# Performance work log

Hardware: AMD Instinct MI355X
Metric: run time of the kernel (lower is better)

The kernel has to match this reference:

```python
import jax, jax.numpy as jnp
import numpy as np

NEIGHBOR_NUM = 4
POOLING_RATE = 4


def setup_inputs() -> dict:
    key = jax.random.key(0)
    k1, k2, k3 = jax.random.split(key, 3)
    B, N, C = 4, 8192, 256
    vertices = jax.random.normal(k1, (B, N, 3), dtype=jnp.float32)
    feature_map = jax.random.normal(k2, (B, N, C), dtype=jnp.float32)
    pool_num = N // POOLING_RATE
    sample_idx = jax.random.permutation(k3, N)[:pool_num].astype(jnp.int32)  # torch.randperm(N)[:pool_num]
    return {"vertices": vertices, "feature_map": feature_map, "radius": 1, "sample_idx": sample_idx}


def _query_ball_point(radius, nsample, xyz):
    # xyz: [B, N, 3]; self-query (new_xyz == xyz)
    B, N, _ = xyz.shape
    sq = jnp.sum(xyz * xyz, axis=-1)                       # [B, N]
    dist = -2.0 * jnp.einsum('bnc,bmc->bnm', xyz, xyz)     # [B, N, N]
    dist = dist + sq[:, :, None] + sq[:, None, :]
    # original code zeroes the diagonal (self-distance)
    diag = jnp.arange(N)
    dist = dist.at[:, diag, diag].set(0.0)
    # mark out-of-ball entries with sentinel N, sort indices, keep first nsample
    idx = jnp.arange(N, dtype=jnp.int32)
    group_idx = jnp.where(dist > radius ** 2, jnp.int32(N), idx[None, None, :])  # [B, N, N]
    group_idx = jnp.sort(group_idx, axis=-1)[:, :, :nsample]                     # [B, N, nsample]
    group_first = group_idx[:, :, :1]
    group_idx = jnp.where(group_idx == N, group_first, group_idx)
    return group_idx


def reference(vertices, feature_map, radius, sample_idx):
    B, N, _ = vertices.shape
    neighbor_index = _query_ball_point(radius, NEIGHBOR_NUM, vertices)          # [B, N, k]
    bidx = jnp.arange(B)[:, None, None]
    neighbor_feature = feature_map[bidx, neighbor_index]                        # [B, N, k, C]
    pooled_feature = jnp.max(neighbor_feature, axis=2)                          # [B, N, C]
    vertices_pool = vertices[:, sample_idx, :]                                  # [B, pool, 3]
    feature_map_pool = pooled_feature[:, sample_idx, :]                         # [B, pool, C]
    return (vertices_pool, feature_map_pool)
```

## Files before the change

kernel.cpp:

```cpp
#include <hip/hip_runtime.h>


#define BB 4
#define NN 8192
#define CC 256
#define PP 2048
#define KK 4
#define SS 1024
#define CH2 16

__device__ __forceinline__ float dist_ref(float xn0, float xn1, float xn2, float sqn,
                                          float x0, float x1, float x2) {
    const float sqm = __fadd_rn(__fadd_rn(__fmul_rn(x0, x0), __fmul_rn(x1, x1)),
                                __fmul_rn(x2, x2));
    const float dot = __fadd_rn(__fadd_rn(__fmul_rn(xn0, x0), __fmul_rn(xn1, x1)),
                                __fmul_rn(xn2, x2));
    return __fadd_rn(__fadd_rn(__fmul_rn(-2.0f, dot), sqn), sqm);
}

__global__ __launch_bounds__(256) void pool_layer_kernel(
    const float* __restrict__ vertices,
    const float* __restrict__ feat,
    const int*   __restrict__ radius_p,
    const int*   __restrict__ sample_idx,
    float* __restrict__ out_v,
    float* __restrict__ out_f)
{
    __shared__ float s_v[SS * 3];

    const int tid  = threadIdx.x;
    const int wave = tid >> 6;
    const int lane = tid & 63;
    const int q    = blockIdx.x * 4 + wave;
    const int b    = q >> 11;
    const int i    = q & (PP - 1);
    const float* vb = vertices + (size_t)b * NN * 3;

    const float4* v4 = (const float4*)vb;
    const float4 st0 = v4[tid];
    const float4 st1 = v4[tid + 256];
    const float4 st2 = v4[tid + 512];

    const int n = sample_idx[i];
    const float xn0 = vb[n * 3 + 0];
    const float xn1 = vb[n * 3 + 1];
    const float xn2 = vb[n * 3 + 2];
    const float sqn = __fadd_rn(__fadd_rn(__fmul_rn(xn0, xn0), __fmul_rn(xn1, xn1)),
                                __fmul_rn(xn2, xn2));
    const int   r  = radius_p[0];
    const float r2 = (float)(r * r);

    ((float4*)s_v)[tid]       = st0;
    ((float4*)s_v)[tid + 256] = st1;
    ((float4*)s_v)[tid + 512] = st2;

    if (lane < 3) out_v[((size_t)b * PP + i) * 3 + lane] = vb[n * 3 + lane];

    __syncthreads();

    int c0 = 0, c1 = 0, c2 = 0, c3 = 0, cnt = 0;
    #pragma unroll
    for (int c = 0; c < SS / 64; ++c) {
        const int m = c * 64 + lane;
        const float x0 = s_v[m * 3 + 0];
        const float x1 = s_v[m * 3 + 1];
        const float x2 = s_v[m * 3 + 2];
        const float dist = dist_ref(xn0, xn1, xn2, sqn, x0, x1, x2);
        unsigned long long mask = __ballot((m == n) || !(dist > r2));
        while (mask && cnt < KK) {
            const int v = c * 64 + (__ffsll(mask) - 1);
            c3 = (cnt == 3) ? v : c3;
            c2 = (cnt == 2) ? v : c2;
            c1 = (cnt == 1) ? v : c1;
            c0 = (cnt == 0) ? v : c0;
            ++cnt;
            mask &= (mask - 1);
        }
    }

    if (cnt < KK) {
        int l0 = NN, l1 = NN, l2 = NN, l3 = NN, lcnt = 0;
        int tot = 0;
        for (int base = 0; base < NN && tot < KK; base += 64 * CH2) {
            float qx[CH2], qy[CH2], qz[CH2];
            #pragma unroll
            for (int c = 0; c < CH2; ++c) {
                const int m = base + c * 64 + lane;
                qx[c] = vb[m * 3 + 0];
                qy[c] = vb[m * 3 + 1];
                qz[c] = vb[m * 3 + 2];
            }
            #pragma unroll
            for (int c = 0; c < CH2; ++c) {
                const int m = base + c * 64 + lane;
                const float dist = dist_ref(xn0, xn1, xn2, sqn, qx[c], qy[c], qz[c]);
                const bool hit = (m == n) || !(dist > r2);
                tot += (int)__popcll(__ballot(hit));
                if (hit && lcnt < KK) {
                    l3 = (lcnt == 3) ? m : l3;
                    l2 = (lcnt == 2) ? m : l2;
                    l1 = (lcnt == 1) ? m : l1;
                    l0 = (lcnt == 0) ? m : l0;
                    ++lcnt;
                }
            }
        }
        int g[KK];
        #pragma unroll
        for (int round = 0; round < KK; ++round) {
            int mmin = l0;
            #pragma unroll
            for (int off = 32; off > 0; off >>= 1)
                mmin = min(mmin, __shfl_xor(mmin, off));
            g[round] = mmin;
            if (l0 == mmin) { l0 = l1; l1 = l2; l2 = l3; l3 = NN; }
        }
        c0 = g[0];
        c1 = (g[1] == NN) ? g[0] : g[1];
        c2 = (g[2] == NN) ? g[0] : g[2];
        c3 = (g[3] == NN) ? g[0] : g[3];
    }

    const float4 a0 = ((const float4*)(feat + ((size_t)b * NN + c0) * CC))[lane];
    const float4 a1 = ((const float4*)(feat + ((size_t)b * NN + c1) * CC))[lane];
    const float4 a2 = ((const float4*)(feat + ((size_t)b * NN + c2) * CC))[lane];
    const float4 a3 = ((const float4*)(feat + ((size_t)b * NN + c3) * CC))[lane];
    float4 o;
    o.x = fmaxf(fmaxf(a0.x, a1.x), fmaxf(a2.x, a3.x));
    o.y = fmaxf(fmaxf(a0.y, a1.y), fmaxf(a2.y, a3.y));
    o.z = fmaxf(fmaxf(a0.z, a1.z), fmaxf(a2.z, a3.z));
    o.w = fmaxf(fmaxf(a0.w, a1.w), fmaxf(a2.w, a3.w));
    ((float4*)(out_f + ((size_t)b * PP + i) * CC))[lane] = o;
}

extern "C" void kernel_launch(void* const* d_in, const int* in_sizes, int n_in,
                              void* d_out, int out_size, void* d_ws, size_t ws_size,
                              hipStream_t stream) {
    const float* vertices   = (const float*)d_in[0];
    const float* feat       = (const float*)d_in[1];
    const int*   radius_p   = (const int*)d_in[2];
    const int*   sample_idx = (const int*)d_in[3];

    float* out_v = (float*)d_out;
    float* out_f = out_v + (size_t)BB * PP * 3;

    dim3 grid(BB * PP / 4), block(256);
    pool_layer_kernel<<<grid, block, 0, stream>>>(
        vertices, feat, radius_p, sample_idx, out_v, out_f);
}
```

Measured before the change: 97.76 us.

## Stage more vertices in LDS and process eight queries per wave

Each block now loads the first 5120 vertices of its batch into shared memory, up from 1024, and each wave handles eight sample queries instead of one. The grid shrinks by a factor of eight, so the cost of staging vertices is spread over 32 queries per block. Queries whose ball has fewer than four hits in the first 1024 points now scan from LDS instead of global memory, and only fall back to global reads beyond 5120. The larger LDS footprint (60 KB) and the 15 float4 staging registers per thread reduce occupancy, and each wave handles its queries one after another.

Measured after the change: 119.7 us. 22.5% more time.

```diff
diff --git a/kernel.cpp b/kernel.cpp
--- a/kernel.cpp
+++ b/kernel.cpp
@@ -6,7 +6,9 @@
 #define CC 256
 #define PP 2048
 #define KK 4
-#define SS 1024
+#define SS 5120
+#define NF4 (SS * 3 / 4)
+#define QPW 8
 #define CH2 16
 
 __device__ __forceinline__ float dist_ref(float xn0, float xn1, float xn2, float sqn,
@@ -31,69 +33,42 @@
     const int tid  = threadIdx.x;
     const int wave = tid >> 6;
     const int lane = tid & 63;
-    const int q    = blockIdx.x * 4 + wave;
-    const int b    = q >> 11;
-    const int i    = q & (PP - 1);
+    const int q0 = blockIdx.x * 32;
+    const int b  = q0 >> 11;
     const float* vb = vertices + (size_t)b * NN * 3;
 
     const float4* v4 = (const float4*)vb;
-    const float4 st0 = v4[tid];
-    const float4 st1 = v4[tid + 256];
-    const float4 st2 = v4[tid + 512];
+    float4 st[15];
+    #pragma unroll
+    for (int k = 0; k < 15; ++k) st[k] = v4[tid + k * 256];
+    #pragma unroll
+    for (int k = 0; k < 15; ++k) ((float4*)s_v)[tid + k * 256] = st[k];
 
-    const int n = sample_idx[i];
-    const float xn0 = vb[n * 3 + 0];
-    const float xn1 = vb[n * 3 + 1];
-    const float xn2 = vb[n * 3 + 2];
-    const float sqn = __fadd_rn(__fadd_rn(__fmul_rn(xn0, xn0), __fmul_rn(xn1, xn1)),
-                                __fmul_rn(xn2, xn2));
     const int   r  = radius_p[0];
     const float r2 = (float)(r * r);
-
-    ((float4*)s_v)[tid]       = st0;
-    ((float4*)s_v)[tid + 256] = st1;
-    ((float4*)s_v)[tid + 512] = st2;
-
-    if (lane < 3) out_v[((size_t)b * PP + i) * 3 + lane] = vb[n * 3 + lane];
-
     __syncthreads();
 
-    int c0 = 0, c1 = 0, c2 = 0, c3 = 0, cnt = 0;
-    #pragma unroll
-    for (int c = 0; c < SS / 64; ++c) {
-        const int m = c * 64 + lane;
-        const float x0 = s_v[m * 3 + 0];
-        const float x1 = s_v[m * 3 + 1];
-        const float x2 = s_v[m * 3 + 2];
-        const float dist = dist_ref(xn0, xn1, xn2, sqn, x0, x1, x2);
-        unsigned long long mask = __ballot((m == n) || !(dist > r2));
-        while (mask && cnt < KK) {
-            const int v = c * 64 + (__ffsll(mask) - 1);
-            c3 = (cnt == 3) ? v : c3;
-            c2 = (cnt == 2) ? v : c2;
-            c1 = (cnt == 1) ? v : c1;
-            c0 = (cnt == 0) ? v : c0;
-            ++cnt;
-            mask &= (mask - 1);
-        }
-    }
+    for (int j = 0; j < QPW; ++j) {
+        const int q = q0 + wave * QPW + j;
+        const int i = q & (PP - 1);
+        const int n = sample_idx[i];
+        const float xn0 = vb[n * 3 + 0];
+        const float xn1 = vb[n * 3 + 1];
+        const float xn2 = vb[n * 3 + 2];
+        const float sqn = __fadd_rn(__fadd_rn(__fmul_rn(xn0, xn0), __fmul_rn(xn1, xn1)),
+                                    __fmul_rn(xn2, xn2));
+        if (lane < 3) out_v[((size_t)b * PP + i) * 3 + lane] = vb[n * 3 + lane];
 
-    if (cnt < KK) {
         int l0 = NN, l1 = NN, l2 = NN, l3 = NN, lcnt = 0;
         int tot = 0;
-        for (int base = 0; base < NN && tot < KK; base += 64 * CH2) {
-            float qx[CH2], qy[CH2], qz[CH2];
+        for (int base = 0; base < SS && tot < KK; base += 1024) {
             #pragma unroll
-            for (int c = 0; c < CH2; ++c) {
+            for (int c = 0; c < 16; ++c) {
                 const int m = base + c * 64 + lane;
-                qx[c] = vb[m * 3 + 0];
-                qy[c] = vb[m * 3 + 1];
-                qz[c] = vb[m * 3 + 2];
-            }
-            #pragma unroll
-            for (int c = 0; c < CH2; ++c) {
-                const int m = base + c * 64 + lane;
-                const float dist = dist_ref(xn0, xn1, xn2, sqn, qx[c], qy[c], qz[c]);
+                const float x0 = s_v[m * 3 + 0];
+                const float x1 = s_v[m * 3 + 1];
+                const float x2 = s_v[m * 3 + 2];
+                const float dist = dist_ref(xn0, xn1, xn2, sqn, x0, x1, x2);
                 const bool hit = (m == n) || !(dist > r2);
                 tot += (int)__popcll(__ballot(hit));
                 if (hit && lcnt < KK) {
@@ -105,6 +80,34 @@
                 }
             }
         }
+
+        if (tot < KK) {
+            for (int base = SS; base < NN && tot < KK; base += 64 * CH2) {
+                float qx[CH2], qy[CH2], qz[CH2];
+                #pragma unroll
+                for (int c = 0; c < CH2; ++c) {
+                    const int m = base + c * 64 + lane;
+                    qx[c] = vb[m * 3 + 0];
+                    qy[c] = vb[m * 3 + 1];
+                    qz[c] = vb[m * 3 + 2];
+                }
+                #pragma unroll
+                for (int c = 0; c < CH2; ++c) {
+                    const int m = base + c * 64 + lane;
+                    const float dist = dist_ref(xn0, xn1, xn2, sqn, qx[c], qy[c], qz[c]);
+                    const bool hit = (m == n) || !(dist > r2);
+                    tot += (int)__popcll(__ballot(hit));
+                    if (hit && lcnt < KK) {
+                        l3 = (lcnt == 3) ? m : l3;
+                        l2 = (lcnt == 2) ? m : l2;
+                        l1 = (lcnt == 1) ? m : l1;
+                        l0 = (lcnt == 0) ? m : l0;
+                        ++lcnt;
+                    }
+                }
+            }
+        }
+
         int g[KK];
         #pragma unroll
         for (int round = 0; round < KK; ++round) {
@@ -115,22 +118,22 @@
             g[round] = mmin;
             if (l0 == mmin) { l0 = l1; l1 = l2; l2 = l3; l3 = NN; }
         }
-        c0 = g[0];
-        c1 = (g[1] == NN) ? g[0] : g[1];
-        c2 = (g[2] == NN) ? g[0] : g[2];
-        c3 = (g[3] == NN) ? g[0] : g[3];
+        const int c0 = g[0];
+        const int c1 = (g[1] == NN) ? g[0] : g[1];
+        const int c2 = (g[2] == NN) ? g[0] : g[2];
+        const int c3 = (g[3] == NN) ? g[0] : g[3];
+
+        const float4 a0 = ((const float4*)(feat + ((size_t)b * NN + c0) * CC))[lane];
+        const float4 a1 = ((const float4*)(feat + ((size_t)b * NN + c1) * CC))[lane];
+        const float4 a2 = ((const float4*)(feat + ((size_t)b * NN + c2) * CC))[lane];
+        const float4 a3 = ((const float4*)(feat + ((size_t)b * NN + c3) * CC))[lane];
+        float4 o;
+        o.x = fmaxf(fmaxf(a0.x, a1.x), fmaxf(a2.x, a3.x));
+        o.y = fmaxf(fmaxf(a0.y, a1.y), fmaxf(a2.y, a3.y));
+        o.z = fmaxf(fmaxf(a0.z, a1.z), fmaxf(a2.z, a3.z));
+        o.w = fmaxf(fmaxf(a0.w, a1.w), fmaxf(a2.w, a3.w));
+        ((float4*)(out_f + ((size_t)b * PP + i) * CC))[lane] = o;
     }
-
-    const float4 a0 = ((const float4*)(feat + ((size_t)b * NN + c0) * CC))[lane];
-    const float4 a1 = ((const float4*)(feat + ((size_t)b * NN + c1) * CC))[lane];
-    const float4 a2 = ((const float4*)(feat + ((size_t)b * NN + c2) * CC))[lane];
-    const float4 a3 = ((const float4*)(feat + ((size_t)b * NN + c3) * CC))[lane];
-    float4 o;
-    o.x = fmaxf(fmaxf(a0.x, a1.x), fmaxf(a2.x, a3.x));
-    o.y = fmaxf(fmaxf(a0.y, a1.y), fmaxf(a2.y, a3.y));
-    o.z = fmaxf(fmaxf(a0.z, a1.z), fmaxf(a2.z, a3.z));
-    o.w = fmaxf(fmaxf(a0.w, a1.w), fmaxf(a2.w, a3.w));
-    ((float4*)(out_f + ((size_t)b * PP + i) * CC))[lane] = o;
 }
 
 extern "C" void kernel_launch(void* const* d_in, const int* in_sizes, int n_in,
@@ -144,7 +147,7 @@
     float* out_v = (float*)d_out;
     float* out_f = out_v + (size_t)BB * PP * 3;
 
-    dim3 grid(BB * PP / 4), block(256);
+    dim3 grid(BB * PP / 32), block(256);
     pool_layer_kernel<<<grid, block, 0, stream>>>(
         vertices, feat, radius_p, sample_idx, out_v, out_f);
 }
```
